# Kernel optimization log

Measured on AMD Instinct MI355X. Metric: run time of the kernel, lower is better.

The kernel has to match this reference:

```python
import jax, jax.numpy as jnp
import numpy as np

LAMBDA_REG = 0.1
EPS = 1e-05


def setup_inputs() -> dict:
    key = jax.random.key(0)
    k1, k2, k3 = jax.random.split(key, 3)
    D, DIM, N = 32, 16, 4096
    A_real = jax.random.normal(k1, (D, DIM, DIM), dtype=jnp.float32)
    A_imag = jax.random.normal(k2, (D, DIM, DIM), dtype=jnp.float32)
    X = jax.random.normal(k3, (N, D), dtype=jnp.float32)
    return {"A_real": A_real, "A_imag": A_imag, "X": X}


def reference(A_real, A_imag, X):
    # A: [D, dim, dim] complex operators; X: [N, D] real positions
    A = (A_real + 1j * A_imag).astype(jnp.complex64)
    N, D = X.shape
    dim = A.shape[-1]
    Xc = X.astype(jnp.complex64)
    I = jnp.eye(dim, dtype=jnp.complex64)

    valid = jnp.isfinite(Xc)                      # [N, D]
    valid_e = valid[:, :, None, None]             # [N, D, 1, 1]
    scaled_I = Xc[:, :, None, None] * I           # [N, D, dim, dim]
    A_exp = A[None, :, :, :]                      # [1, D, dim, dim] (broadcast over N)
    scaled_I_clean = jnp.where(valid_e, scaled_I, A_exp)
    H_diff = jnp.where(valid_e, A_exp - scaled_I_clean, 0.0)  # [N, D, dim, dim]

    # 0.5 * sum_d H_diff @ H_diff^H  (Hermitian by construction)
    H = 0.5 * jnp.einsum('ndij,ndkj->nik', H_diff, jnp.conj(H_diff))
    H = H + EPS * I                               # [N, dim, dim]

    eigvals, eigvecs = jnp.linalg.eigh(H)
    psi0 = eigvecs[:, :, 0]                       # ground state, [N, dim]
    phase = psi0[:, 0] / jnp.abs(psi0[:, 0])
    psi0 = psi0 / phase[:, None]
    projector = psi0[:, :, None] * jnp.conj(psi0)[:, None, :]  # [N, dim, dim]

    # Faithful to torch.einsum('ndij,njk->nd', ...): sums over i, j AND k
    position = jnp.einsum('dij,njk->nd', A, projector).real    # [N, D]
    A2 = jnp.matmul(A, A)                                       # [D, dim, dim]
    expectation_A2 = jnp.einsum('dij,njk->nd', A2, projector).real
    variance = jnp.sum(expectation_A2 - position ** 2)

    position_error = jnp.sum((position - X) ** 2)
    loss = (position_error + LAMBDA_REG * variance) / N
    return loss
```

## Files before the change

kernel.cpp:

```cpp
#include <hip/hip_runtime.h>

#define NS 4096
#define DC 32
#define MAXROUND 210
#define CHKIV 8

typedef float v2f __attribute__((ext_vector_type(2)));

#define CFENCE() asm volatile("" ::: "memory")

static __device__ __forceinline__ v2f vswap(v2f b) {
    return __builtin_shufflevector(b, b, 1, 0);
}

static __device__ __forceinline__ int slot_of(int r, int rr) {
    if (r == 15) return 0;
    int m = r - rr; if (m < 0) m += 15;
    if (m == 0) return 1;
    return (m <= 7) ? 2*m : 31 - 2*m;
}
static __device__ __forceinline__ int pi_next(int s) {
    if (s == 0) return 0;
    if (s == 2) return 1;
    if (!(s & 1)) return s - 2;
    return (s == 15) ? 14 : s + 2;
}
static __device__ __forceinline__ int kmix(int sr) {
    return ((sr >> 1) ^ ((sr & 1) << 2)) & 7;
}
static __device__ __forceinline__ int laddr(int sr, int sc) {
    return (sr << 7) | ((((sc >> 1) ^ kmix(sr)) & 7) << 4) | ((sc & 1) << 3);
}

static __device__ __forceinline__ float4 make_rot(float4 f0, float4 f1) {
    float av = f0.x, dv = f1.z;
    float ab2 = f0.z*f0.z + f0.w*f0.w;
    float c_, s_, er, ei;
    if (ab2 > 1e-60f) {
        float abr = __builtin_amdgcn_rsqf(ab2);
        er = f0.z * abr; ei = f0.w * abr;
        float tau = (dv - av) * (0.5f * abr);
        float den = fabsf(tau) + sqrtf(1.f + tau*tau);
        float tv = __builtin_amdgcn_rcpf(den);
        tv = (tau < 0.f) ? -tv : tv;
        c_ = __builtin_amdgcn_rsqf(1.f + tv*tv);
        s_ = tv * c_;
    } else { c_ = 1.f; s_ = 0.f; er = 1.f; ei = 0.f; }
    return make_float4(c_, s_, er, ei);
}

static __device__ __forceinline__ void rot_quartet(
    float4 fa, float4 fb,
    float4 f0, float4 f1, float4 g0, float4 g1,
    v2f& n11, v2f& n12, v2f& n21, v2f& n22,
    v2f& u11, v2f& u12, v2f& u21, v2f& u22)
{
    v2f h11 = {f0.x, f0.y}, h12 = {f0.z, f0.w};
    v2f h21 = {f1.x, f1.y}, h22 = {f1.z, f1.w};
    v2f q11 = {g0.x, g0.y}, q12 = {g0.z, g0.w};
    v2f q21 = {g1.x, g1.y}, q22 = {g1.z, g1.w};

    const float cb = fb.x, sb = fb.y, ebx = fb.z, eby = fb.w;
    const float sbex = sb*ebx, sbey = sb*eby;
    const float cbex = cb*ebx, cbey = cb*eby;
    const v2f CB  = {cb, cb},      SB  = {sb, sb};
    const v2f P1x = {-sbex,-sbex}, P1y = {-sbey, sbey};
    const v2f Q1x = {cbex, cbex},  Q1y = {cbey,-cbey};
    const float ca = fa.x, sa = fa.y, eax = fa.z, eay = fa.w;
    const float saex = sa*eax, saey = sa*eay;
    const float caex = ca*eax, caey = ca*eay;
    const v2f CA  = {ca, ca},      SA  = {sa, sa};
    const v2f P2x = {-saex,-saex}, P2y = {saey,-saey};
    const v2f Q2x = {caex, caex},  Q2y = {-caey, caey};

    v2f t11 = CB*h11  + P1x*h12 + P1y*vswap(h12);
    v2f t12 = Q1x*h12 + Q1y*vswap(h12) + SB*h11;
    v2f t21 = CB*h21  + P1x*h22 + P1y*vswap(h22);
    v2f t22 = Q1x*h22 + Q1y*vswap(h22) + SB*h21;
    n11 = CA*t11  + P2x*t21 + P2y*vswap(t21);
    n12 = CA*t12  + P2x*t22 + P2y*vswap(t22);
    n21 = Q2x*t21 + Q2y*vswap(t21) + SA*t11;
    n22 = Q2x*t22 + Q2y*vswap(t22) + SA*t12;
    u11 = CB*q11  + P1x*q12 + P1y*vswap(q12);
    u12 = Q1x*q12 + Q1y*vswap(q12) + SB*q11;
    u21 = CB*q21  + P1x*q22 + P1y*vswap(q22);
    u22 = Q1x*q22 + Q1y*vswap(q22) + SB*q21;
}

__global__ __launch_bounds__(256) void precompute_kernel(
    const float* __restrict__ Ar, const float* __restrict__ Ai,
    float2* __restrict__ S, float2* __restrict__ W,
    float2* __restrict__ cA, float2* __restrict__ cA2,
    float* __restrict__ out)
{
    const int d = blockIdx.x;
    const int t = threadIdx.x;
    if (d == 0 && t == 0) out[0] = 0.f;
    const int i = t >> 4, j = t & 15;
    __shared__ float ar[16][16], ai[16][16], a2r[16][16], a2i[16][16];
    ar[i][j] = Ar[d*256 + t];
    ai[i][j] = Ai[d*256 + t];
    __syncthreads();
    float a2re = 0.f, a2im = 0.f, wre = 0.f, wim = 0.f;
    for (int k = 0; k < 16; ++k) {
        float xr = ar[i][k], xi = ai[i][k];
        a2re += xr*ar[k][j] - xi*ai[k][j];
        a2im += xr*ai[k][j] + xi*ar[k][j];
        wre += xr*ar[j][k] + xi*ai[j][k];
        wim += xi*ar[j][k] - xr*ai[j][k];
    }
    S[d*256 + t] = make_float2(ar[i][j] + ar[j][i], ai[i][j] - ai[j][i]);
    W[d*256 + t] = make_float2(wre, wim);
    a2r[i][j] = a2re; a2i[i][j] = a2im;
    __syncthreads();
    if (t < 16) {
        float sr = 0.f, si = 0.f, s2r = 0.f, s2i = 0.f;
        for (int ii = 0; ii < 16; ++ii) {
            sr  += ar[ii][t];  si  += ai[ii][t];
            s2r += a2r[ii][t]; s2i += a2i[ii][t];
        }
        cA [d*16 + t] = make_float2(sr,  si);
        cA2[d*16 + t] = make_float2(s2r, s2i);
    }
}

__global__ __launch_bounds__(64) void energy_kernel(
    const float* __restrict__ X,
    const float2* __restrict__ S, const float2* __restrict__ W,
    const float2* __restrict__ cA, const float2* __restrict__ cA2,
    float* __restrict__ out)
{
    const int n0 = blockIdx.x * 2;
    const int t = threadIdx.x;
    const int a = t >> 3, b = t & 7;

    __shared__ __align__(16) v2f H[2][256], V[2][256];
    __shared__ float4 csco[2][8];
    __shared__ float  xS[2][32];
    __shared__ float  diagS[2][16];
    __shared__ v2f    psiS[2][16];
    __shared__ int    midxS[2];

    const float* XA = X + n0*DC;
    const float* XB = X + (n0 + 1)*DC;
    if (t < 32) { xS[0][t] = XA[t]; xS[1][t] = XB[t]; }

    const int sr0 = 2*a, sr1 = 2*a + 1;
    const int sc0 = 2*b, sc1 = 2*b + 1;
    const int rd0 = (sr0 << 7) | (((b ^ kmix(sr0)) & 7) << 4);
    const int rd1 = (sr1 << 7) | (((b ^ kmix(sr1)) & 7) << 4);
    const int pr0 = pi_next(sr0), pr1 = pi_next(sr1);
    const int pc0 = pi_next(sc0), pc1 = pi_next(sc1);
    const int wH00 = laddr(pr0, pc0), wH01 = laddr(pr0, pc1);
    const int wH10 = laddr(pr1, pc0), wH11 = laddr(pr1, pc1);
    const int wV00 = laddr(sr0, pc0), wV01 = laddr(sr0, pc1);
    const int wV10 = laddr(sr1, pc0), wV11 = laddr(sr1, pc1);
    const bool diagLane = (a == b);

    float invTolA, invTolB;
    {
        const int bi = t >> 2, bj = (t & 3) * 4, e0 = t * 4;
        v2f accA[4] = {{0.f,0.f},{0.f,0.f},{0.f,0.f},{0.f,0.f}};
        v2f accB[4] = {{0.f,0.f},{0.f,0.f},{0.f,0.f},{0.f,0.f}};
        float sxa = 0.f, sxb = 0.f;
        for (int d = 0; d < DC; ++d) {
            float xa = XA[d], xb = XB[d];
            sxa += xa*xa; sxb += xb*xb;
            const float4* w4 = (const float4*)(W + d*256 + e0);
            const float4* s4 = (const float4*)(S + d*256 + e0);
            float4 wa = w4[0], wb = w4[1];
            float4 sa = s4[0], sb = s4[1];
            v2f xva = {xa, xa}, xvb = {xb, xb};
            accA[0] += (v2f){wa.x, wa.y} - xva * (v2f){sa.x, sa.y};
            accA[1] += (v2f){wa.z, wa.w} - xva * (v2f){sa.z, sa.w};
            accA[2] += (v2f){wb.x, wb.y} - xva * (v2f){sb.x, sb.y};
            accA[3] += (v2f){wb.z, wb.w} - xva * (v2f){sb.z, sb.w};
            accB[0] += (v2f){wa.x, wa.y} - xvb * (v2f){sa.x, sa.y};
            accB[1] += (v2f){wa.z, wa.w} - xvb * (v2f){sa.z, sa.w};
            accB[2] += (v2f){wb.x, wb.y} - xvb * (v2f){sb.x, sb.y};
            accB[3] += (v2f){wb.z, wb.w} - xvb * (v2f){sb.z, sb.w};
        }
        float sdA = 0.5f*sxa + 1e-5f;
        float sdB = 0.5f*sxb + 1e-5f;
        float nfA = 0.f, nfB = 0.f;
        const int sbi = slot_of(bi, 0);
        #pragma unroll
        for (int u = 0; u < 4; ++u) {
            int j = bj + u;
            v2f hA = 0.5f * accA[u];
            v2f hB = 0.5f * accB[u];
            if (bi == j) { hA.x += sdA; hB.x += sdB; }
            nfA += hA.x*hA.x + hA.y*hA.y;
            nfB += hB.x*hB.x + hB.y*hB.y;
            const int scj = slot_of(j, 0);
            *(v2f*)((char*)H + laddr(sbi, scj)) = hA;
            *(v2f*)((char*)H + 2048 + laddr(sbi, scj)) = hB;
            v2f iv = (bi == j) ? (v2f){1.f, 0.f} : (v2f){0.f, 0.f};
            *(v2f*)((char*)V + laddr(bi, scj)) = iv;
            *(v2f*)((char*)V + 2048 + laddr(bi, scj)) = iv;
        }
        #pragma unroll
        for (int m = 1; m < 64; m <<= 1) {
            nfA += __shfl_xor(nfA, m);
            nfB += __shfl_xor(nfB, m);
        }
        invTolA = __builtin_amdgcn_rcpf(1e-10f * nfA);
        invTolB = __builtin_amdgcn_rcpf(1e-10f * nfB);
    }
    __syncthreads();

    int rr = 0, iter = 0, chkcd = CHKIV;
    for (;;) {
        const char* Hc = (const char*)H;
        const char* Vc = (const char*)V;
        float4 f0A = *(const float4*)(Hc + rd0);
        float4 f1A = *(const float4*)(Hc + rd1);
        float4 f0B = *(const float4*)(Hc + 2048 + rd0);
        float4 f1B = *(const float4*)(Hc + 2048 + rd1);
        float4 g0A = *(const float4*)(Vc + rd0);
        float4 g1A = *(const float4*)(Vc + rd1);
        float4 g0B = *(const float4*)(Vc + 2048 + rd0);
        float4 g1B = *(const float4*)(Vc + 2048 + rd1);

        if (diagLane) {
            csco[0][a] = make_rot(f0A, f1A);
            csco[1][a] = make_rot(f0B, f1B);
        }
        CFENCE();

        float4 faA = csco[0][a], fbA = csco[0][b];
        float4 faB = csco[1][a], fbB = csco[1][b];

        v2f n11A, n12A, n21A, n22A, u11A, u12A, u21A, u22A;
        v2f n11B, n12B, n21B, n22B, u11B, u12B, u21B, u22B;
        rot_quartet(faA, fbA, f0A, f1A, g0A, g1A,
                    n11A, n12A, n21A, n22A, u11A, u12A, u21A, u22A);
        rot_quartet(faB, fbB, f0B, f1B, g0B, g1B,
                    n11B, n12B, n21B, n22B, u11B, u12B, u21B, u22B);

        char* Hw = (char*)H;
        char* Vw = (char*)V;
        *(v2f*)(Hw + wH00) = n11A;
        *(v2f*)(Hw + wH01) = n12A;
        *(v2f*)(Hw + wH10) = n21A;
        *(v2f*)(Hw + wH11) = n22A;
        *(v2f*)(Vw + wV00) = u11A;
        *(v2f*)(Vw + wV01) = u12A;
        *(v2f*)(Vw + wV10) = u21A;
        *(v2f*)(Vw + wV11) = u22A;
        *(v2f*)(Hw + 2048 + wH00) = n11B;
        *(v2f*)(Hw + 2048 + wH01) = n12B;
        *(v2f*)(Hw + 2048 + wH10) = n21B;
        *(v2f*)(Hw + 2048 + wH11) = n22B;
        *(v2f*)(Vw + 2048 + wV00) = u11B;
        *(v2f*)(Vw + 2048 + wV01) = u12B;
        *(v2f*)(Vw + 2048 + wV10) = u21B;
        *(v2f*)(Vw + 2048 + wV11) = u22B;
        CFENCE();

        rr = (rr == 14) ? 0 : rr + 1;
        ++iter;
        if (chkcd == 1) {
            float oA = n12A.x*n12A.x + n12A.y*n12A.y + n21A.x*n21A.x + n21A.y*n21A.y;
            float oB = n12B.x*n12B.x + n12B.y*n12B.y + n21B.x*n21B.x + n21B.y*n21B.y;
            if (!diagLane) {
                oA += n11A.x*n11A.x + n11A.y*n11A.y + n22A.x*n22A.x + n22A.y*n22A.y;
                oB += n11B.x*n11B.x + n11B.y*n11B.y + n22B.x*n22B.x + n22B.y*n22B.y;
            }
            oA *= invTolA; oB *= invTolB;
            #pragma unroll
            for (int m = 1; m < 64; m <<= 1) {
                oA += __shfl_xor(oA, m);
                oB += __shfl_xor(oB, m);
            }
            if (fmaxf(oA, oB) < 1.f || iter >= MAXROUND) break;
            chkcd = CHKIV;
        } else { --chkcd; }
    }
    __syncthreads();

    const int rrx = rr;
    if (t < 32) {
        const int s = t >> 4, r = t & 15;
        const int sd = slot_of(r, rrx);
        diagS[s][r] = (*(const v2f*)((const char*)H + s*2048 + laddr(sd, sd))).x;
    }
    __syncthreads();
    if ((t & 31) == 0) {
        const int s = t >> 5;
        float best = diagS[s][0]; int bi_ = 0;
        for (int m = 1; m < 16; ++m) {
            float vv = diagS[s][m];
            if (vv < best) { best = vv; bi_ = m; }
        }
        midxS[s] = bi_;
    }
    __syncthreads();
    if (t < 32) {
        const int s = t >> 4, r = t & 15;
        const int sm = slot_of(midxS[s], rrx);
        psiS[s][r] = *(const v2f*)((const char*)V + s*2048 + laddr(r, sm));
    }
    __syncthreads();

    float contrib;
    {
        const int s = t >> 5, d = t & 31;
        float tr = 0.f, ti = 0.f;
        v2f psi[16];
        for (int jj = 0; jj < 16; ++jj) {
            psi[jj] = psiS[s][jj];
            tr += psi[jj].x; ti += psi[jj].y;
        }
        float zr = 0.f, zi = 0.f, z2r = 0.f, z2i = 0.f;
        for (int jj = 0; jj < 16; ++jj) {
            float2 cj  = cA [d*16 + jj];
            float2 c2j = cA2[d*16 + jj];
            zr  += cj.x*psi[jj].x  - cj.y*psi[jj].y;
            zi  += cj.x*psi[jj].y  + cj.y*psi[jj].x;
            z2r += c2j.x*psi[jj].x - c2j.y*psi[jj].y;
            z2i += c2j.x*psi[jj].y + c2j.y*psi[jj].x;
        }
        float pos = zr*tr + zi*ti;
        float e2  = z2r*tr + z2i*ti;
        float dx  = pos - xS[s][d];
        contrib = dx*dx + 0.1f*(e2 - pos*pos);
    }
    #pragma unroll
    for (int m = 1; m < 64; m <<= 1)
        contrib += __shfl_xor(contrib, m);
    if (t == 0) atomicAdd(out, contrib * (1.0f/(float)NS));
}

extern "C" void kernel_launch(void* const* d_in, const int* in_sizes, int n_in,
                              void* d_out, int out_size, void* d_ws, size_t ws_size,
                              hipStream_t stream)
{
    const float* A_real = (const float*)d_in[0];
    const float* A_imag = (const float*)d_in[1];
    const float* X      = (const float*)d_in[2];
    float* out = (float*)d_out;

    float2* S   = (float2*)d_ws;
    float2* W   = S  + DC*256;
    float2* cA  = W  + DC*256;
    float2* cA2 = cA + DC*16;
    (void)in_sizes; (void)n_in; (void)out_size; (void)ws_size;

    precompute_kernel<<<DC, 256, 0, stream>>>(A_real, A_imag, S, W, cA, cA2, out);
    energy_kernel<<<NS/2, 64, 0, stream>>>(X, S, W, cA, cA2, out);
}
```

Baseline: 149.8 us.

## Keep eigenvector matrix in registers and permute columns with DPP

The eigenvector accumulator V in the Jacobi sweep loop now stays in registers instead of shared memory. The column permutation between rounds is done with DPP row shifts and lane-dependent selects. This removes eight LDS reads and eight LDS writes per round per lane. In exchange it adds more registers, DPP moves and selects, plus a write of V to LDS after convergence. Correctness depends on the DPP shift pattern matching the old pi_next column permutation.

```diff
diff --git a/kernel.cpp b/kernel.cpp
--- a/kernel.cpp
+++ b/kernel.cpp
@@ -11,6 +11,21 @@
 
 static __device__ __forceinline__ v2f vswap(v2f b) {
     return __builtin_shufflevector(b, b, 1, 0);
+}
+
+static __device__ __forceinline__ float dpp_from_hi(float x) {
+    return __int_as_float(__builtin_amdgcn_update_dpp(
+        0, __float_as_int(x), 0x101, 0xf, 0xf, true));
+}
+static __device__ __forceinline__ float dpp_from_lo(float x) {
+    return __int_as_float(__builtin_amdgcn_update_dpp(
+        0, __float_as_int(x), 0x111, 0xf, 0xf, true));
+}
+static __device__ __forceinline__ v2f dpp2_from_hi(v2f v) {
+    return (v2f){dpp_from_hi(v.x), dpp_from_hi(v.y)};
+}
+static __device__ __forceinline__ v2f dpp2_from_lo(v2f v) {
+    return (v2f){dpp_from_lo(v.x), dpp_from_lo(v.y)};
 }
 
 static __device__ __forceinline__ int slot_of(int r, int rr) {
@@ -51,14 +66,12 @@
 
 static __device__ __forceinline__ void rot_quartet(
     float4 fa, float4 fb,
-    float4 f0, float4 f1, float4 g0, float4 g1,
+    float4 f0, float4 f1, v2f q11, v2f q12, v2f q21, v2f q22,
     v2f& n11, v2f& n12, v2f& n21, v2f& n22,
     v2f& u11, v2f& u12, v2f& u21, v2f& u22)
 {
     v2f h11 = {f0.x, f0.y}, h12 = {f0.z, f0.w};
     v2f h21 = {f1.x, f1.y}, h22 = {f1.z, f1.w};
-    v2f q11 = {g0.x, g0.y}, q12 = {g0.z, g0.w};
-    v2f q21 = {g1.x, g1.y}, q22 = {g1.z, g1.w};
 
     const float cb = fb.x, sb = fb.y, ebx = fb.z, eby = fb.w;
     const float sbex = sb*ebx, sbey = sb*eby;
@@ -87,6 +100,21 @@
     u22 = Q1x*q22 + Q1y*vswap(q22) + SB*q21;
 }
 
+static __device__ __forceinline__ void v_advance(
+    bool b0, bool b7,
+    v2f u11, v2f u12, v2f u21, v2f u22,
+    v2f& q11, v2f& q12, v2f& q21, v2f& q22)
+{
+    v2f s11 = dpp2_from_hi(u11);
+    v2f s21 = dpp2_from_hi(u21);
+    v2f l12 = dpp2_from_lo(u12);
+    v2f l22 = dpp2_from_lo(u22);
+    q11 = b7 ? u12 : (b0 ? u11 : s11);
+    q21 = b7 ? u22 : (b0 ? u21 : s21);
+    q12 = b0 ? s11 : l12;
+    q22 = b0 ? s21 : l22;
+}
+
 __global__ __launch_bounds__(256) void precompute_kernel(
     const float* __restrict__ Ar, const float* __restrict__ Ai,
     float2* __restrict__ S, float2* __restrict__ W,
@@ -134,8 +162,9 @@
     const int t = threadIdx.x;
     const int a = t >> 3, b = t & 7;
 
-    __shared__ __align__(16) v2f H[2][256], V[2][256];
+    __shared__ __align__(16) v2f H[2][256];
     __shared__ float4 csco[2][8];
+    __shared__ float4 vS[2][16][8];
     __shared__ float  xS[2][32];
     __shared__ float  diagS[2][16];
     __shared__ v2f    psiS[2][16];
@@ -153,9 +182,16 @@
     const int pc0 = pi_next(sc0), pc1 = pi_next(sc1);
     const int wH00 = laddr(pr0, pc0), wH01 = laddr(pr0, pc1);
     const int wH10 = laddr(pr1, pc0), wH11 = laddr(pr1, pc1);
-    const int wV00 = laddr(sr0, pc0), wV01 = laddr(sr0, pc1);
-    const int wV10 = laddr(sr1, pc0), wV11 = laddr(sr1, pc1);
     const bool diagLane = (a == b);
+    const bool b0 = (b == 0), b7 = (b == 7);
+
+    const int j0 = b0 ? 15 : b;
+    const int j1 = b0 ? 0  : 15 - b;
+    v2f qA11 = {(sr0 == j0) ? 1.f : 0.f, 0.f};
+    v2f qA12 = {(sr0 == j1) ? 1.f : 0.f, 0.f};
+    v2f qA21 = {(sr1 == j0) ? 1.f : 0.f, 0.f};
+    v2f qA22 = {(sr1 == j1) ? 1.f : 0.f, 0.f};
+    v2f qB11 = qA11, qB12 = qA12, qB21 = qA21, qB22 = qA22;
 
     float invTolA, invTolB;
     {
@@ -195,9 +231,6 @@
             const int scj = slot_of(j, 0);
             *(v2f*)((char*)H + laddr(sbi, scj)) = hA;
             *(v2f*)((char*)H + 2048 + laddr(sbi, scj)) = hB;
-            v2f iv = (bi == j) ? (v2f){1.f, 0.f} : (v2f){0.f, 0.f};
-            *(v2f*)((char*)V + laddr(bi, scj)) = iv;
-            *(v2f*)((char*)V + 2048 + laddr(bi, scj)) = iv;
         }
         #pragma unroll
         for (int m = 1; m < 64; m <<= 1) {
@@ -212,15 +245,10 @@
     int rr = 0, iter = 0, chkcd = CHKIV;
     for (;;) {
         const char* Hc = (const char*)H;
-        const char* Vc = (const char*)V;
         float4 f0A = *(const float4*)(Hc + rd0);
         float4 f1A = *(const float4*)(Hc + rd1);
         float4 f0B = *(const float4*)(Hc + 2048 + rd0);
         float4 f1B = *(const float4*)(Hc + 2048 + rd1);
-        float4 g0A = *(const float4*)(Vc + rd0);
-        float4 g1A = *(const float4*)(Vc + rd1);
-        float4 g0B = *(const float4*)(Vc + 2048 + rd0);
-        float4 g1B = *(const float4*)(Vc + 2048 + rd1);
 
         if (diagLane) {
             csco[0][a] = make_rot(f0A, f1A);
@@ -233,29 +261,23 @@
 
         v2f n11A, n12A, n21A, n22A, u11A, u12A, u21A, u22A;
         v2f n11B, n12B, n21B, n22B, u11B, u12B, u21B, u22B;
-        rot_quartet(faA, fbA, f0A, f1A, g0A, g1A,
+        rot_quartet(faA, fbA, f0A, f1A, qA11, qA12, qA21, qA22,
                     n11A, n12A, n21A, n22A, u11A, u12A, u21A, u22A);
-        rot_quartet(faB, fbB, f0B, f1B, g0B, g1B,
+        rot_quartet(faB, fbB, f0B, f1B, qB11, qB12, qB21, qB22,
                     n11B, n12B, n21B, n22B, u11B, u12B, u21B, u22B);
 
         char* Hw = (char*)H;
-        char* Vw = (char*)V;
         *(v2f*)(Hw + wH00) = n11A;
         *(v2f*)(Hw + wH01) = n12A;
         *(v2f*)(Hw + wH10) = n21A;
         *(v2f*)(Hw + wH11) = n22A;
-        *(v2f*)(Vw + wV00) = u11A;
-        *(v2f*)(Vw + wV01) = u12A;
-        *(v2f*)(Vw + wV10) = u21A;
-        *(v2f*)(Vw + wV11) = u22A;
         *(v2f*)(Hw + 2048 + wH00) = n11B;
         *(v2f*)(Hw + 2048 + wH01) = n12B;
         *(v2f*)(Hw + 2048 + wH10) = n21B;
         *(v2f*)(Hw + 2048 + wH11) = n22B;
-        *(v2f*)(Vw + 2048 + wV00) = u11B;
-        *(v2f*)(Vw + 2048 + wV01) = u12B;
-        *(v2f*)(Vw + 2048 + wV10) = u21B;
-        *(v2f*)(Vw + 2048 + wV11) = u22B;
+
+        v_advance(b0, b7, u11A, u12A, u21A, u22A, qA11, qA12, qA21, qA22);
+        v_advance(b0, b7, u11B, u12B, u21B, u22B, qB11, qB12, qB21, qB22);
         CFENCE();
 
         rr = (rr == 14) ? 0 : rr + 1;
@@ -277,6 +299,11 @@
             chkcd = CHKIV;
         } else { --chkcd; }
     }
+
+    vS[0][sr0][b] = make_float4(qA11.x, qA11.y, qA12.x, qA12.y);
+    vS[0][sr1][b] = make_float4(qA21.x, qA21.y, qA22.x, qA22.y);
+    vS[1][sr0][b] = make_float4(qB11.x, qB11.y, qB12.x, qB12.y);
+    vS[1][sr1][b] = make_float4(qB21.x, qB21.y, qB22.x, qB22.y);
     __syncthreads();
 
     const int rrx = rr;
@@ -299,7 +326,8 @@
     if (t < 32) {
         const int s = t >> 4, r = t & 15;
         const int sm = slot_of(midxS[s], rrx);
-        psiS[s][r] = *(const v2f*)((const char*)V + s*2048 + laddr(r, sm));
+        float4 f4 = vS[s][r][sm >> 1];
+        psiS[s][r] = (sm & 1) ? (v2f){f4.z, f4.w} : (v2f){f4.x, f4.y};
     }
     __syncthreads();
 
```

After: 143.5 us. -4.2%, faster.
